# Kernel tuning notes

Hardware: AMD Instinct MI355X
Metric: run time of the kernel (lower is better)

Reference implementation:

```python
import jax, jax.numpy as jnp
import numpy as np

CHW = (1, 256, 256)
NPH, NPW = 16, 16
NB = 8          # n_blocks
D = 384         # hidden_d
H = 6           # n_heads
DH = D // H     # d_head = 64
OUT = 4
PH, PW = CHW[1] // NPH, CHW[2] // NPW
IN_D = CHW[0] * PH * PW        # 256
S = NPH * NPW + 1              # 257 tokens (CLS + patches)
EPS = 1e-5                     # torch LayerNorm default


def positional_embeddings(seq_len, d):
    # matches get_positional_embeddings: sin(i/10000^(j/d)) even j, cos(i/10000^((j-1)/d)) odd j
    i = jnp.arange(seq_len, dtype=jnp.float32)[:, None]
    j = jnp.arange(d, dtype=jnp.float32)[None, :]
    j_eff = jnp.where(j % 2 == 0, j, j - 1)
    ang = i / jnp.power(jnp.float32(10000.0), j_eff / d)
    return jnp.where(j % 2 == 0, jnp.sin(ang), jnp.cos(ang))


def patchify(images):
    # (n,c,h,w) -> (n, NPH*NPW, c*PH*PW), patch flattened channel-first like patch.flatten()
    n, c, h, w = images.shape
    x = images.reshape(n, c, NPH, PH, NPW, PW)
    x = x.transpose(0, 2, 4, 1, 3, 5)  # n, nph, npw, c, ph, pw
    return x.reshape(n, NPH * NPW, c * PH * PW)


def layernorm(x, g, b):
    mu = jnp.mean(x, axis=-1, keepdims=True)
    var = jnp.mean(jnp.square(x - mu), axis=-1, keepdims=True)
    return (x - mu) * jax.lax.rsqrt(var + EPS) * g + b


def mhsa(x, Wq, bq, Wk, bk, Wv, bv):
    # x: [B,S,D]; W*: [H,DH,DH] (torch Linear convention out=x@W.T+b), b*: [H,DH]
    B = x.shape[0]
    xh = x.reshape(B, S, H, DH)
    q = jnp.einsum('bshd,hed->bshe', xh, Wq) + bq
    k = jnp.einsum('bshd,hed->bshe', xh, Wk) + bk
    v = jnp.einsum('bshd,hed->bshe', xh, Wv) + bv
    scores = jnp.einsum('bqhe,bkhe->bhqk', q, k) / jnp.float32(DH) ** 0.5
    attn = jax.nn.softmax(scores, axis=-1)
    o = jnp.einsum('bhqk,bkhe->bqhe', attn, v)
    return o.reshape(B, S, D)


def setup_inputs() -> dict:
    key = jax.random.key(0)
    ks = jax.random.split(key, 24)
    s = 0.02
    B = 64
    inp = {
        'images': jax.random.normal(ks[0], (B, *CHW), jnp.float32),
        'Wmap': jax.random.normal(ks[1], (D, IN_D), jnp.float32) * s,
        'bmap': jax.random.normal(ks[2], (D,), jnp.float32) * s,
        'cls': jax.random.uniform(ks[3], (1, D), jnp.float32),
        'ln1_g': jnp.ones((NB, D), jnp.float32),
        'ln1_b': jnp.zeros((NB, D), jnp.float32),
        'Wq': jax.random.normal(ks[4], (NB, H, DH, DH), jnp.float32) * s,
        'bq': jax.random.normal(ks[5], (NB, H, DH), jnp.float32) * s,
        'Wk': jax.random.normal(ks[6], (NB, H, DH, DH), jnp.float32) * s,
        'bk': jax.random.normal(ks[7], (NB, H, DH), jnp.float32) * s,
        'Wv': jax.random.normal(ks[8], (NB, H, DH, DH), jnp.float32) * s,
        'bv': jax.random.normal(ks[9], (NB, H, DH), jnp.float32) * s,
        'ln2_g': jnp.ones((NB, D), jnp.float32),
        'ln2_b': jnp.zeros((NB, D), jnp.float32),
        'W1': jax.random.normal(ks[10], (NB, 4 * D, D), jnp.float32) * s,
        'b1': jax.random.normal(ks[11], (NB, 4 * D), jnp.float32) * s,
        'W2': jax.random.normal(ks[12], (NB, D, 4 * D), jnp.float32) * s,
        'b2': jax.random.normal(ks[13], (NB, D), jnp.float32) * s,
        'Wout': jax.random.normal(ks[14], (OUT, D), jnp.float32) * s,
        'bout': jax.random.normal(ks[15], (OUT,), jnp.float32) * s,
    }
    return inp


def reference(images, Wmap, bmap, cls, ln1_g, ln1_b, Wq, bq, Wk, bk, Wv, bv,
              ln2_g, ln2_b, W1, b1, W2, b2, Wout, bout):
    B = images.shape[0]
    patches = patchify(images)                        # [B, S-1, IN_D]
    tokens = patches @ Wmap.T + bmap                  # [B, S-1, D]
    tokens = jnp.concatenate([jnp.broadcast_to(cls[None], (B, 1, D)), tokens], axis=1)
    out = tokens + positional_embeddings(S, D)[None]  # [B, S, D]
    for blk in range(NB):
        out = out + mhsa(layernorm(out, ln1_g[blk], ln1_b[blk]),
                         Wq[blk], bq[blk], Wk[blk], bk[blk], Wv[blk], bv[blk])
        h = layernorm(out, ln2_g[blk], ln2_b[blk])
        h = jax.nn.gelu(h @ W1[blk].T + b1[blk], approximate=False)
        out = out + (h @ W2[blk].T + b2[blk])
    cls_out = out[:, 0]                               # [B, D]
    return jax.nn.softmax(cls_out @ Wout.T + bout, axis=-1)
```

## Files before the change

kernel.cpp:

```cpp
#include <hip/hip_runtime.h>

typedef __bf16 bf16x8 __attribute__((ext_vector_type(8)));
typedef float f32x4 __attribute__((ext_vector_type(4)));
typedef unsigned short u16;
typedef unsigned short u16x4 __attribute__((ext_vector_type(4)));

typedef __attribute__((address_space(3))) unsigned int as3_u32;
typedef __attribute__((address_space(1))) unsigned int as1_u32;

static __device__ __forceinline__ float b2f(u16 u) {
    union { unsigned int ui; float f; } v; v.ui = ((unsigned int)u) << 16; return v.f;
}
static __device__ __forceinline__ u16 f2b(float f) {
    union { float f; unsigned int u; } v; v.f = f;
    unsigned int r = v.u + 0x7FFFu + ((v.u >> 16) & 1u);
    return (u16)(r >> 16);
}
static __device__ __forceinline__ float h2f(u16 u) {
    union { u16 u; _Float16 h; } v; v.u = u; return (float)v.h;
}
static __device__ __forceinline__ u16 f2h(float f) {
    union { u16 u; _Float16 h; } v; v.h = (_Float16)f; return v.u;
}
static __device__ __forceinline__ float pos_emb(int s, int d) {
    int je = d & ~1;
    float ang = (float)s * powf(10000.0f, -(float)je / 384.0f);
    return (d & 1) ? cosf(ang) : sinf(ang);
}
static __device__ __forceinline__ float gelu_f(float x) {
    float xs = x * 0.70710678118654752f;
    float ax = fabsf(xs);
    float t = __builtin_amdgcn_rcpf(1.0f + 0.3275911f * ax);
    float poly = ((((1.061405429f * t - 1.453152027f) * t + 1.421413741f) * t
                   - 0.284496736f) * t + 0.254829592f) * t;
    float e = __expf(-ax * ax);
    float erfv = 1.0f - poly * e;
    erfv = (xs < 0.f) ? -erfv : erfv;
    return 0.5f * x * (1.0f + erfv);
}
static __device__ __forceinline__ void async16(const void* g, void* l) {
    __builtin_amdgcn_global_load_lds((const as1_u32*)g, (as3_u32*)l, 16, 0, 0);
}

#define MFMA16 __builtin_amdgcn_mfma_f32_16x16x32_bf16

static __device__ __forceinline__ bf16x8 ln8(const u16* __restrict__ p, float mu, float rs,
                                             f32x4 g0, f32x4 g1, f32x4 b0, f32x4 b1) {
    u16x4 xlo = *(const u16x4*)p;
    u16x4 xhi = *(const u16x4*)(p + 4);
    u16 o[8];
#pragma unroll
    for (int j = 0; j < 4; j++) o[j]     = f2b((h2f(xlo[j]) - mu) * rs * g0[j] + b0[j]);
#pragma unroll
    for (int j = 0; j < 4; j++) o[4 + j] = f2b((h2f(xhi[j]) - mu) * rs * g1[j] + b1[j]);
    return *(bf16x8*)o;
}

template<int K>
static __device__ __forceinline__ void stage_tile(const u16* __restrict__ gbase,
                                                  u16* lds, int kt, int t) {
#pragma unroll
    for (int j = 0; j < 4; j++) {
        int o = j * 4096 + t * 16;
        int row = o >> 7;
        int c = (o >> 4) & 7;
        int gc = c ^ (row & 7);
        const u16* src = gbase + (size_t)row * K + kt * 64 + gc * 8;
        async16(src, (char*)lds + o);
    }
}

template<int K, int EPI>
__global__ __launch_bounds__(256) void k_gemm128(const u16* __restrict__ A,
                                                 const u16* __restrict__ Bw,
                                                 const float* __restrict__ bias,
                                                 u16* __restrict__ out16,
                                                 u16* __restrict__ xres) {
    __shared__ u16 lds[2][128 * 64];
    const int t = threadIdx.x;
    const int NY = gridDim.y;
    int nwg = gridDim.x * NY;
    int flat = blockIdx.x + gridDim.x * blockIdx.y;
    int q8 = nwg >> 3, r8 = nwg & 7, xcd = flat & 7, idx = flat >> 3;
    int wg = (xcd < r8 ? xcd * (q8 + 1) : r8 * (q8 + 1) + (xcd - r8) * q8) + idx;
    const int mt = wg / NY, nt = wg - mt * NY;

    const u16* Ab = A + (size_t)mt * 128 * K;
    const u16* Bb = Bw + (size_t)nt * 128 * K;
    constexpr int NKT = K / 64;
    const int lane = t & 63, w = t >> 6;
    const int wm = (w >> 1) * 64, wn = (w & 1) * 64;
    const int r = lane & 15, g = lane >> 4;

    f32x4 acc[4][4] = {};
    for (int kt = 0; kt < NKT; kt++) {
        stage_tile<K>(Ab, lds[0], kt, t);
        stage_tile<K>(Bb, lds[1], kt, t);
        asm volatile("s_waitcnt vmcnt(0)" ::: "memory");
        __builtin_amdgcn_sched_barrier(0);
        __builtin_amdgcn_s_barrier();
        __builtin_amdgcn_sched_barrier(0);
#pragma unroll
        for (int ks = 0; ks < 2; ks++) {
            bf16x8 a[4], b[4];
#pragma unroll
            for (int i = 0; i < 4; i++) {
                int ra = wm + i * 16 + r;
                int ca = (ks * 4 + g) ^ (ra & 7);
                a[i] = *(const bf16x8*)((const char*)lds[0] + ra * 128 + ca * 16);
                int rb = wn + i * 16 + r;
                int cb = (ks * 4 + g) ^ (rb & 7);
                b[i] = *(const bf16x8*)((const char*)lds[1] + rb * 128 + cb * 16);
            }
            __builtin_amdgcn_s_setprio(1);
#pragma unroll
            for (int i = 0; i < 4; i++)
#pragma unroll
                for (int jj = 0; jj < 4; jj++)
                    acc[i][jj] = MFMA16(a[i], b[jj], acc[i][jj], 0, 0, 0);
            __builtin_amdgcn_s_setprio(0);
        }
        __builtin_amdgcn_s_barrier();
    }
#pragma unroll
    for (int i = 0; i < 4; i++) {
#pragma unroll
        for (int q = 0; q < 4; q++) {
            int ml = mt * 128 + wm + i * 16 + g * 4 + q;
#pragma unroll
            for (int jj = 0; jj < 4; jj++) {
                int n = nt * 128 + wn + jj * 16 + r;
                float v = acc[i][jj][q] + bias[n];
                if (EPI == 0) {
                    out16[(size_t)ml * 1536 + n] = f2b(gelu_f(v));
                } else {
                    if (ml < 16448) {
                        size_t o = (size_t)ml * 384 + n;
                        xres[o] = f2h(h2f(xres[o]) + v);
                    }
                }
            }
        }
    }
}

__global__ __launch_bounds__(64) void k_fattn(const u16* __restrict__ qb,
                                              const u16* __restrict__ kb,
                                              const u16* __restrict__ vT,
                                              u16* __restrict__ ao) {
    __shared__ u16 pl[32][40];
    const int lane = threadIdx.x;
    int flat = blockIdx.x;
    int xcd = flat & 7, idx = flat >> 3;
    int lbh = idx / 9;
    const int bh = xcd * 48 + lbh;
    const int q0 = (idx - lbh * 9) * 32;
    const int b = bh / 6, h = bh - b * 6;
    const int r = lane & 15, g = lane >> 4;

    const u16* qbase = qb + ((size_t)b * 257) * 384 + h * 64;
    const u16* kbase = kb + ((size_t)b * 257) * 384 + h * 64;
    const u16* vbase = vT + ((size_t)bh * 64) * 288;

    bf16x8 qf[2][2];
#pragma unroll
    for (int ti = 0; ti < 2; ti++)
#pragma unroll
        for (int kh = 0; kh < 2; kh++)
            qf[ti][kh] = *(const bf16x8*)(qbase + (size_t)(q0 + ti * 16 + r) * 384 + kh * 32 + g * 8);

    f32x4 accO[2][2][2] = {};
    f32x4 sum_[2] = {};

    for (int kv0 = 0; kv0 < 288; kv0 += 32) {
        bf16x8 kf[2][2];
#pragma unroll
        for (int tj = 0; tj < 2; tj++)
#pragma unroll
            for (int kh = 0; kh < 2; kh++)
                kf[tj][kh] = *(const bf16x8*)(kbase + (size_t)(kv0 + tj * 16 + r) * 384 + kh * 32 + g * 8);
        bf16x8 vf[2][2];
#pragma unroll
        for (int eT = 0; eT < 2; eT++)
#pragma unroll
            for (int tjE = 0; tjE < 2; tjE++)
                vf[eT][tjE] = *(const bf16x8*)(vbase + (size_t)(eT * 32 + tjE * 16 + r) * 288 + kv0 + g * 8);

        f32x4 s_[2][2] = {};
#pragma unroll
        for (int ti = 0; ti < 2; ti++)
#pragma unroll
            for (int tj = 0; tj < 2; tj++) {
                s_[ti][tj] = MFMA16(qf[ti][0], kf[tj][0], s_[ti][tj], 0, 0, 0);
                s_[ti][tj] = MFMA16(qf[ti][1], kf[tj][1], s_[ti][tj], 0, 0, 0);
            }
#pragma unroll
        for (int ti = 0; ti < 2; ti++) {
#pragma unroll
            for (int tj = 0; tj < 2; tj++) {
                bool bad = (kv0 + tj * 16 + r) >= 257;
#pragma unroll
                for (int q = 0; q < 4; q++) {
                    float p = bad ? 0.f : __expf(s_[ti][tj][q] * 0.125f);
                    s_[ti][tj][q] = p;
                }
                sum_[ti] += s_[ti][tj];
#pragma unroll
                for (int q = 0; q < 4; q++)
                    pl[ti * 16 + g * 4 + q][tj * 16 + r] = f2b(s_[ti][tj][q]);
            }
        }
        bf16x8 pa[2];
#pragma unroll
        for (int ti2 = 0; ti2 < 2; ti2++)
            pa[ti2] = *(const bf16x8*)&pl[ti2 * 16 + r][g * 8];
#pragma unroll
        for (int eT = 0; eT < 2; eT++)
#pragma unroll
            for (int ti2 = 0; ti2 < 2; ti2++)
#pragma unroll
                for (int tjE = 0; tjE < 2; tjE++)
                    accO[eT][ti2][tjE] = MFMA16(pa[ti2], vf[eT][tjE], accO[eT][ti2][tjE], 0, 0, 0);
    }
#pragma unroll
    for (int o = 1; o < 16; o <<= 1)
#pragma unroll
        for (int ti = 0; ti < 2; ti++)
#pragma unroll
            for (int q = 0; q < 4; q++)
                sum_[ti][q] += __shfl_xor(sum_[ti][q], o, 64);
#pragma unroll
    for (int ti = 0; ti < 2; ti++)
#pragma unroll
        for (int q = 0; q < 4; q++) {
            int qi = q0 + ti * 16 + g * 4 + q;
            if (qi < 257) {
                float inv = 1.0f / sum_[ti][q];
                u16* pao = ao + ((size_t)b * 257 + qi) * 384 + h * 64;
#pragma unroll
                for (int eT = 0; eT < 2; eT++)
#pragma unroll
                    for (int tjE = 0; tjE < 2; tjE++)
                        pao[eT * 32 + tjE * 16 + r] = f2b(accO[eT][ti][tjE][q] * inv);
            }
        }
}

__global__ __launch_bounds__(256) void k_cvt16(const void* __restrict__ src, u16* __restrict__ dst,
                                               int n, const unsigned* __restrict__ probe) {
    const bool isf32 = (*probe == 0x3F800000u);
    int i0 = (blockIdx.x * 256 + threadIdx.x) * 4;
    if (isf32) {
        const float* s = (const float*)src;
#pragma unroll
        for (int j = 0; j < 4; j++) { int i = i0 + j; if (i < n) dst[i] = f2b(s[i]); }
    } else {
        const u16* s = (const u16*)src;
#pragma unroll
        for (int j = 0; j < 4; j++) { int i = i0 + j; if (i < n) dst[i] = s[i]; }
    }
}
__global__ __launch_bounds__(256) void k_cvt32(const void* __restrict__ src, float* __restrict__ dst,
                                               int n, const unsigned* __restrict__ probe) {
    const bool isf32 = (*probe == 0x3F800000u);
    int i0 = (blockIdx.x * 256 + threadIdx.x) * 4;
    if (isf32) {
        const float* s = (const float*)src;
#pragma unroll
        for (int j = 0; j < 4; j++) { int i = i0 + j; if (i < n) dst[i] = s[i]; }
    } else {
        const u16* s = (const u16*)src;
#pragma unroll
        for (int j = 0; j < 4; j++) { int i = i0 + j; if (i < n) dst[i] = b2f(s[i]); }
    }
}

__global__ __launch_bounds__(256) void k_vtpad(u16* __restrict__ vT) {
    int idx = blockIdx.x * 256 + threadIdx.x;
    const int total = 384 * 64 * 31;
    if (idx < total) {
        int be = idx / 31; int s = 257 + (idx - be * 31);
        vT[(size_t)be * 288 + s] = 0;
    }
}

__global__ __launch_bounds__(256) void k_patch(const u16* __restrict__ img,
                                               const u16* __restrict__ Wmap,
                                               const float* __restrict__ bmap,
                                               u16* __restrict__ x) {
    const int lane = threadIdx.x & 63;
    const int wv = threadIdx.x >> 6;
    const int mt = blockIdx.x * 4 + wv;
    const int nt = blockIdx.y;
    const int m0 = mt * 32, n0 = nt * 32;
    const int r = lane & 15, kr = (lane >> 4) << 3;
    f32x4 acc[2][2] = {};
    int ma = m0 + r;
    size_t base0 = (size_t)(ma >> 8) * 65536 + (size_t)((ma >> 4) & 15) * 4096 + (size_t)(ma & 15) * 16;
    ma += 16;
    size_t base1 = (size_t)(ma >> 8) * 65536 + (size_t)((ma >> 4) & 15) * 4096 + (size_t)(ma & 15) * 16;
    const u16* pb0 = Wmap + (size_t)(n0 + r) * 256 + kr;
    const u16* pb1 = pb0 + 16 * 256;
    for (int k0 = 0; k0 < 256; k0 += 32) {
        int k = k0 + kr;
        size_t off = (size_t)(k >> 4) * 256 + (k & 15);
        bf16x8 a0 = *(const bf16x8*)(img + base0 + off);
        bf16x8 a1 = *(const bf16x8*)(img + base1 + off);
        bf16x8 b0 = *(const bf16x8*)(pb0 + k0);
        bf16x8 b1 = *(const bf16x8*)(pb1 + k0);
        acc[0][0] = MFMA16(a0, b0, acc[0][0], 0, 0, 0);
        acc[0][1] = MFMA16(a0, b1, acc[0][1], 0, 0, 0);
        acc[1][0] = MFMA16(a1, b0, acc[1][0], 0, 0, 0);
        acc[1][1] = MFMA16(a1, b1, acc[1][1], 0, 0, 0);
    }
#pragma unroll
    for (int ti = 0; ti < 2; ti++)
#pragma unroll
        for (int i = 0; i < 4; i++) {
            int m = m0 + ti * 16 + ((lane >> 4) << 2) + i;
            int b = m >> 8, p = m & 255, s = p + 1;
            u16* px = x + ((size_t)b * 257 + s) * 384;
#pragma unroll
            for (int tj = 0; tj < 2; tj++) {
                int n = n0 + tj * 16 + (lane & 15);
                px[n] = f2h(acc[ti][tj][i] + bmap[n] + pos_emb(s, n));
            }
        }
}

__global__ __launch_bounds__(384) void k_cls(const float* __restrict__ cls, u16* __restrict__ x) {
    int b = blockIdx.x, d = threadIdx.x;
    x[(size_t)b * 257 * 384 + d] = f2h(cls[d] + pos_emb(0, d));
}

__global__ __launch_bounds__(256) void k_stats(const u16* __restrict__ x,
                                               float* __restrict__ st) {
    const int lane = threadIdx.x & 63, wv = threadIdx.x >> 6;
    const int row = blockIdx.x * 16 + wv * 4 + (lane >> 4);
    const int r = lane & 15;
    const u16* px = x + (size_t)row * 384;
    f32x4 v[6]; float s = 0.f;
#pragma unroll
    for (int i = 0; i < 6; i++) {
        u16x4 x4 = *(const u16x4*)(px + i * 64 + r * 4);
#pragma unroll
        for (int j = 0; j < 4; j++) v[i][j] = h2f(x4[j]);
        s += v[i][0] + v[i][1] + v[i][2] + v[i][3];
    }
#pragma unroll
    for (int o = 1; o < 16; o <<= 1) s += __shfl_xor(s, o, 64);
    float mu = s * (1.0f / 384.0f);
    float q = 0.f;
#pragma unroll
    for (int i = 0; i < 6; i++)
#pragma unroll
        for (int j = 0; j < 4; j++) { float d = v[i][j] - mu; q += d * d; }
#pragma unroll
    for (int o = 1; o < 16; o <<= 1) q += __shfl_xor(q, o, 64);
    float rstd = rsqrtf(q * (1.0f / 384.0f) + 1e-5f);
    if (r == 0) { st[row * 2] = mu; st[row * 2 + 1] = rstd; }
}

__global__ __launch_bounds__(256) void k_ln2r(u16* __restrict__ x,
                                              const u16* __restrict__ ao,
                                              const float* __restrict__ g,
                                              const float* __restrict__ bb,
                                              u16* __restrict__ xn) {
    const int lane = threadIdx.x & 63, wv = threadIdx.x >> 6;
    const int row = blockIdx.x * 16 + wv * 4 + (lane >> 4);
    const int r = lane & 15;
    u16* px = x + (size_t)row * 384;
    const u16* pa = ao + (size_t)row * 384;
    f32x4 v[6]; float s = 0.f;
#pragma unroll
    for (int i = 0; i < 6; i++) {
        u16x4 x4 = *(const u16x4*)(px + i * 64 + r * 4);
        u16x4 a4 = *(const u16x4*)(pa + i * 64 + r * 4);
#pragma unroll
        for (int j = 0; j < 4; j++) v[i][j] = h2f(x4[j]) + b2f(a4[j]);
        s += v[i][0] + v[i][1] + v[i][2] + v[i][3];
    }
#pragma unroll
    for (int o = 1; o < 16; o <<= 1) s += __shfl_xor(s, o, 64);
    float mu = s * (1.0f / 384.0f);
    float q = 0.f;
#pragma unroll
    for (int i = 0; i < 6; i++)
#pragma unroll
        for (int j = 0; j < 4; j++) { float d = v[i][j] - mu; q += d * d; }
#pragma unroll
    for (int o = 1; o < 16; o <<= 1) q += __shfl_xor(q, o, 64);
    float rstd = rsqrtf(q * (1.0f / 384.0f) + 1e-5f);
    u16* po = xn + (size_t)row * 384;
#pragma unroll
    for (int i = 0; i < 6; i++) {
        int d0 = i * 64 + r * 4;
        u16x4 h4;
#pragma unroll
        for (int j = 0; j < 4; j++) h4[j] = f2h(v[i][j]);
        *(u16x4*)(px + d0) = h4;
        f32x4 gg = *(const f32x4*)(g + d0);
        f32x4 bv = *(const f32x4*)(bb + d0);
        u16x4 o4;
#pragma unroll
        for (int j = 0; j < 4; j++) o4[j] = f2b((v[i][j] - mu) * rstd * gg[j] + bv[j]);
        *(u16x4*)(po + d0) = o4;
    }
}

__global__ __launch_bounds__(256) void k_qkv3(const u16* __restrict__ x,
                                              const float* __restrict__ st,
                                              const float* __restrict__ lg,
                                              const float* __restrict__ lb,
                                              const u16* __restrict__ Wq,
                                              const u16* __restrict__ Wk,
                                              const u16* __restrict__ Wv,
                                              const float* __restrict__ bq,
                                              const float* __restrict__ bk,
                                              const float* __restrict__ bv,
                                              u16* __restrict__ qo,
                                              u16* __restrict__ ko,
                                              u16* __restrict__ vT) {
    const int lane = threadIdx.x & 63, wv = threadIdx.x >> 6;
    int nwg = 129 * 12;
    int flat = blockIdx.x + 129 * blockIdx.y;
    int q8 = nwg >> 3, r8 = nwg & 7, xcd = flat & 7, idx = flat >> 3;
    int wg = (xcd < r8 ? xcd * (q8 + 1) : r8 * (q8 + 1) + (xcd - r8) * q8) + idx;
    int bxx = wg / 12, rest = wg - bxx * 12;

    const int mt = bxx * 4 + wv; if (mt >= 514) return;
    const int nt = rest & 1, h = rest >> 1;
    const int r = lane & 15, kr = (lane >> 4) << 3;

    const int row0 = mt * 32 + r, row1 = row0 + 16;
    const u16* xr0 = x + (size_t)row0 * 384 + h * 64;
    const u16* xr1 = x + (size_t)row1 * 384 + h * 64;
    const float mu0 = st[row0 * 2], rs0 = st[row0 * 2 + 1];
    const float mu1 = st[row1 * 2], rs1 = st[row1 * 2 + 1];
    f32x4 gA = *(const f32x4*)(lg + h * 64 + kr);
    f32x4 gB = *(const f32x4*)(lg + h * 64 + kr + 4);
    f32x4 gC = *(const f32x4*)(lg + h * 64 + 32 + kr);
    f32x4 gD = *(const f32x4*)(lg + h * 64 + 32 + kr + 4);
    f32x4 bA = *(const f32x4*)(lb + h * 64 + kr);
    f32x4 bB = *(const f32x4*)(lb + h * 64 + kr + 4);
    f32x4 bC = *(const f32x4*)(lb + h * 64 + 32 + kr);
    f32x4 bD = *(const f32x4*)(lb + h * 64 + 32 + kr + 4);

    bf16x8 a00 = ln8(xr0 + kr, mu0, rs0, gA, gB, bA, bB);
    bf16x8 a10 = ln8(xr1 + kr, mu1, rs1, gA, gB, bA, bB);
    bf16x8 a01 = ln8(xr0 + 32 + kr, mu0, rs0, gC, gD, bC, bD);
    bf16x8 a11 = ln8(xr1 + 32 + kr, mu1, rs1, gC, gD, bC, bD);

    const u16* Ws[3] = { Wq, Wk, Wv };
    const float* bs[3] = { bq, bk, bv };
#pragma unroll
    for (int ty = 0; ty < 3; ty++) {
        const u16* Bb = Ws[ty] + ((size_t)h * 64 + nt * 32) * 64;
        bf16x8 b00 = *(const bf16x8*)(Bb + (size_t)r * 64 + kr);
        bf16x8 b10 = *(const bf16x8*)(Bb + (size_t)(16 + r) * 64 + kr);
        bf16x8 b01 = *(const bf16x8*)(Bb + (size_t)r * 64 + 32 + kr);
        bf16x8 b11 = *(const bf16x8*)(Bb + (size_t)(16 + r) * 64 + 32 + kr);
        f32x4 acc[2][2] = {};
        acc[0][0] = MFMA16(a00, b00, acc[0][0], 0, 0, 0);
        acc[0][1] = MFMA16(a00, b10, acc[0][1], 0, 0, 0);
        acc[1][0] = MFMA16(a10, b00, acc[1][0], 0, 0, 0);
        acc[1][1] = MFMA16(a10, b10, acc[1][1], 0, 0, 0);
        acc[0][0] = MFMA16(a01, b01, acc[0][0], 0, 0, 0);
        acc[0][1] = MFMA16(a01, b11, acc[0][1], 0, 0, 0);
        acc[1][0] = MFMA16(a11, b01, acc[1][0], 0, 0, 0);
        acc[1][1] = MFMA16(a11, b11, acc[1][1], 0, 0, 0);
        const float* bias = bs[ty];
#pragma unroll
        for (int ti = 0; ti < 2; ti++)
#pragma unroll
            for (int i = 0; i < 4; i++) {
                int m = mt * 32 + ti * 16 + ((lane >> 4) << 2) + i;
#pragma unroll
                for (int tj = 0; tj < 2; tj++) {
                    int nl = nt * 32 + tj * 16 + (lane & 15);
                    float v = acc[ti][tj][i] + bias[h * 64 + nl];
                    if (ty == 0) {
                        qo[(size_t)m * 384 + h * 64 + nl] = f2b(v);
                    } else if (ty == 1) {
                        ko[(size_t)m * 384 + h * 64 + nl] = f2b(v);
                    } else {
                        int b = m / 257, s = m - b * 257;
                        vT[(((size_t)b * 6 + h) * 64 + nl) * 288 + s] = f2b(v);
                    }
                }
            }
    }
}

__global__ __launch_bounds__(256) void k_head(const u16* __restrict__ x,
                                              const float* __restrict__ Wout,
                                              const float* __restrict__ bout,
                                              float* __restrict__ out) {
    int t = threadIdx.x; int b = t >> 2, o = t & 3;
    const u16* px = x + (size_t)b * 257 * 384;
    const float* pw = Wout + o * 384;
    float s = 0.f;
    for (int d = 0; d < 384; d++) s += h2f(px[d]) * pw[d];
    s += bout[o];
    float mx = fmaxf(s, __shfl_xor(s, 1, 4));
    mx = fmaxf(mx, __shfl_xor(mx, 2, 4));
    float e = expf(s - mx);
    float sm = e + __shfl_xor(e, 1, 4);
    sm += __shfl_xor(sm, 2, 4);
    out[t] = e / sm;
}

extern "C" void kernel_launch(void* const* d_in, const int* in_sizes, int n_in,
                              void* d_out, int out_size, void* d_ws, size_t ws_size,
                              hipStream_t stream) {
    const unsigned* probe = (const unsigned*)d_in[4];

    char* w = (char*)d_ws;
    size_t used = 0;
    auto alloc = [&](size_t bytes) -> char* {
        char* p = w + used; used += (bytes + 255) & ~(size_t)255; return p;
    };
    u16*   x   = (u16*)  alloc(16448ull * 384 * 2);
    u16*   xn  = (u16*)  alloc(16512ull * 384 * 2);
    u16*   qb  = (u16*)  alloc(16448ull * 384 * 2);
    u16*   kb  = (u16*)  alloc(16448ull * 384 * 2);
    u16*   vT  = (u16*)  alloc(384ull * 64 * 288 * 2);
    u16*   ao  = (u16*)  alloc(16448ull * 384 * 2);
    float* stx = (float*)alloc(16448ull * 2 * 4);
    u16*   imB = (u16*)  alloc(4194304ull * 2);
    u16*   WmB = (u16*)  alloc(98304ull * 2);
    u16*   WqB = (u16*)  alloc(196608ull * 2);
    u16*   WkB = (u16*)  alloc(196608ull * 2);
    u16*   WvB = (u16*)  alloc(196608ull * 2);
    u16*   W1B = (u16*)  alloc(4718592ull * 2);
    u16*   W2B = (u16*)  alloc(4718592ull * 2);
    float* prm = (float*)alloc(39172ull * 4);
    u16*   hb  = (u16*)  alloc(16512ull * 1536 * 2);
    (void)ws_size;

    float* bmapF = prm + 0;
    float* clsF  = prm + 384;
    float* ln1gF = prm + 768;
    float* ln1bF = prm + 3840;
    float* bqF   = prm + 6912;
    float* bkF   = prm + 9984;
    float* bvF   = prm + 13056;
    float* ln2gF = prm + 16128;
    float* ln2bF = prm + 19200;
    float* b1F   = prm + 22272;
    float* b2F   = prm + 34560;
    float* WoutF = prm + 37632;
    float* boutF = prm + 39168;

    dim3 B256(256);
    auto cvt16 = [&](const void* src, u16* dst, int n) {
        hipLaunchKernelGGL(k_cvt16, dim3((n + 1023) / 1024), B256, 0, stream, src, dst, n, probe);
    };
    auto cvt32 = [&](const void* src, float* dst, int n) {
        hipLaunchKernelGGL(k_cvt32, dim3((n + 1023) / 1024), B256, 0, stream, src, dst, n, probe);
    };
    cvt16(d_in[0],  imB, 4194304);
    cvt16(d_in[1],  WmB, 98304);
    cvt16(d_in[6],  WqB, 196608);
    cvt16(d_in[8],  WkB, 196608);
    cvt16(d_in[10], WvB, 196608);
    cvt16(d_in[14], W1B, 4718592);
    cvt16(d_in[16], W2B, 4718592);
    cvt32(d_in[2],  bmapF, 384);
    cvt32(d_in[3],  clsF,  384);
    cvt32(d_in[4],  ln1gF, 3072);
    cvt32(d_in[5],  ln1bF, 3072);
    cvt32(d_in[7],  bqF,   3072);
    cvt32(d_in[9],  bkF,   3072);
    cvt32(d_in[11], bvF,   3072);
    cvt32(d_in[12], ln2gF, 3072);
    cvt32(d_in[13], ln2bF, 3072);
    cvt32(d_in[15], b1F,   12288);
    cvt32(d_in[17], b2F,   3072);
    cvt32(d_in[18], WoutF, 1536);
    cvt32(d_in[19], boutF, 4);
    (void)in_sizes; (void)n_in; (void)out_size;

    hipMemsetAsync(xn + 16448ull * 384, 0, 64ull * 384 * 2, stream);

    hipLaunchKernelGGL(k_vtpad, dim3((384 * 64 * 31 + 255) / 256), B256, 0, stream, vT);
    hipLaunchKernelGGL(k_patch, dim3(128, 12), B256, 0, stream, imB, WmB, bmapF, x);
    hipLaunchKernelGGL(k_cls, dim3(64), dim3(384), 0, stream, clsF, x);
    for (int blk = 0; blk < 8; blk++) {
        hipLaunchKernelGGL(k_stats, dim3(1028), B256, 0, stream, x, stx);
        hipLaunchKernelGGL(k_qkv3, dim3(129, 12), B256, 0, stream, x, stx,
                           ln1gF + blk * 384, ln1bF + blk * 384,
                           WqB + (size_t)blk * 24576, WkB + (size_t)blk * 24576, WvB + (size_t)blk * 24576,
                           bqF + blk * 384, bkF + blk * 384, bvF + blk * 384,
                           qb, kb, vT);
        hipLaunchKernelGGL(k_fattn, dim3(3456), dim3(64), 0, stream, qb, kb, vT, ao);
        hipLaunchKernelGGL(k_ln2r, dim3(1028), B256, 0, stream, x, ao,
                           ln2gF + blk * 384, ln2bF + blk * 384, xn);
        k_gemm128<384, 0><<<dim3(129, 12), B256, 0, stream>>>(
            xn, W1B + (size_t)blk * 1536 * 384, b1F + blk * 1536, hb, nullptr);
        k_gemm128<1536, 1><<<dim3(129, 3), B256, 0, stream>>>(
            hb, W2B + (size_t)blk * 384 * 1536, b2F + blk * 384, nullptr, x);
    }
    hipLaunchKernelGGL(k_head, dim3(1), B256, 0, stream, x, WoutF, boutF, (float*)d_out);
}
```

Measured before the change: 1.341 ms.

## Compute only CLS token rows in the final transformer block

In the last block only the CLS token's output feeds the classification head. The attention query side, LN2+residual, and the MLP are therefore restricted to the 64 CLS rows through a CLS-mode attention launch, a small ln2 kernel writing a compact buffer, and a new GEMM epilogue that scatters back to the CLS rows. K/V for all tokens are still computed, so attention remains exact. This cuts roughly seven-eighths of the last block's attention-output and MLP work but adds code paths and a padded compact buffer.

```diff
diff --git a/kernel.cpp b/kernel.cpp
--- a/kernel.cpp
+++ b/kernel.cpp
@@ -133,9 +133,14 @@
                 float v = acc[i][jj][q] + bias[n];
                 if (EPI == 0) {
                     out16[(size_t)ml * 1536 + n] = f2b(gelu_f(v));
-                } else {
+                } else if (EPI == 1) {
                     if (ml < 16448) {
                         size_t o = (size_t)ml * 384 + n;
+                        xres[o] = f2h(h2f(xres[o]) + v);
+                    }
+                } else {
+                    if (ml < 64) {
+                        size_t o = ((size_t)ml * 257) * 384 + n;
                         xres[o] = f2h(h2f(xres[o]) + v);
                     }
                 }
@@ -147,14 +152,19 @@
 __global__ __launch_bounds__(64) void k_fattn(const u16* __restrict__ qb,
                                               const u16* __restrict__ kb,
                                               const u16* __restrict__ vT,
-                                              u16* __restrict__ ao) {
+                                              u16* __restrict__ ao, int clsmode) {
     __shared__ u16 pl[32][40];
     const int lane = threadIdx.x;
     int flat = blockIdx.x;
-    int xcd = flat & 7, idx = flat >> 3;
-    int lbh = idx / 9;
-    const int bh = xcd * 48 + lbh;
-    const int q0 = (idx - lbh * 9) * 32;
+    int bh, q0;
+    if (clsmode) {
+        bh = flat; q0 = 0;
+    } else {
+        int xcd = flat & 7, idx = flat >> 3;
+        int lbh = idx / 9;
+        bh = xcd * 48 + lbh;
+        q0 = (idx - lbh * 9) * 32;
+    }
     const int b = bh / 6, h = bh - b * 6;
     const int r = lane & 15, g = lane >> 4;
 
@@ -408,6 +418,54 @@
     }
 }
 
+__global__ __launch_bounds__(256) void k_ln2r_cls(u16* __restrict__ x,
+                                                  const u16* __restrict__ ao,
+                                                  const float* __restrict__ g,
+                                                  const float* __restrict__ bb,
+                                                  u16* __restrict__ xnc) {
+    const int lane = threadIdx.x & 63, wv = threadIdx.x >> 6;
+    const int bi = blockIdx.x * 16 + wv * 4 + (lane >> 4);
+    const int r = lane & 15;
+    const size_t row = (size_t)bi * 257;
+    u16* px = x + row * 384;
+    const u16* pa = ao + row * 384;
+    f32x4 v[6]; float s = 0.f;
+#pragma unroll
+    for (int i = 0; i < 6; i++) {
+        u16x4 x4 = *(const u16x4*)(px + i * 64 + r * 4);
+        u16x4 a4 = *(const u16x4*)(pa + i * 64 + r * 4);
+#pragma unroll
+        for (int j = 0; j < 4; j++) v[i][j] = h2f(x4[j]) + b2f(a4[j]);
+        s += v[i][0] + v[i][1] + v[i][2] + v[i][3];
+    }
+#pragma unroll
+    for (int o = 1; o < 16; o <<= 1) s += __shfl_xor(s, o, 64);
+    float mu = s * (1.0f / 384.0f);
+    float q = 0.f;
+#pragma unroll
+    for (int i = 0; i < 6; i++)
+#pragma unroll
+        for (int j = 0; j < 4; j++) { float d = v[i][j] - mu; q += d * d; }
+#pragma unroll
+    for (int o = 1; o < 16; o <<= 1) q += __shfl_xor(q, o, 64);
+    float rstd = rsqrtf(q * (1.0f / 384.0f) + 1e-5f);
+    u16* po = xnc + (size_t)bi * 384;
+#pragma unroll
+    for (int i = 0; i < 6; i++) {
+        int d0 = i * 64 + r * 4;
+        u16x4 h4;
+#pragma unroll
+        for (int j = 0; j < 4; j++) h4[j] = f2h(v[i][j]);
+        *(u16x4*)(px + d0) = h4;
+        f32x4 gg = *(const f32x4*)(g + d0);
+        f32x4 bv = *(const f32x4*)(bb + d0);
+        u16x4 o4;
+#pragma unroll
+        for (int j = 0; j < 4; j++) o4[j] = f2b((v[i][j] - mu) * rstd * gg[j] + bv[j]);
+        *(u16x4*)(po + d0) = o4;
+    }
+}
+
 __global__ __launch_bounds__(256) void k_qkv3(const u16* __restrict__ x,
                                               const float* __restrict__ st,
                                               const float* __restrict__ lg,
@@ -522,6 +580,7 @@
     };
     u16*   x   = (u16*)  alloc(16448ull * 384 * 2);
     u16*   xn  = (u16*)  alloc(16512ull * 384 * 2);
+    u16*   xnc = (u16*)  alloc(128ull * 384 * 2);
     u16*   qb  = (u16*)  alloc(16448ull * 384 * 2);
     u16*   kb  = (u16*)  alloc(16448ull * 384 * 2);
     u16*   vT  = (u16*)  alloc(384ull * 64 * 288 * 2);
@@ -582,6 +641,7 @@
     (void)in_sizes; (void)n_in; (void)out_size;
 
     hipMemsetAsync(xn + 16448ull * 384, 0, 64ull * 384 * 2, stream);
+    hipMemsetAsync(xnc + 64ull * 384, 0, 64ull * 384 * 2, stream);
 
     hipLaunchKernelGGL(k_vtpad, dim3((384 * 64 * 31 + 255) / 256), B256, 0, stream, vT);
     hipLaunchKernelGGL(k_patch, dim3(128, 12), B256, 0, stream, imB, WmB, bmapF, x);
@@ -593,13 +653,23 @@
                            WqB + (size_t)blk * 24576, WkB + (size_t)blk * 24576, WvB + (size_t)blk * 24576,
                            bqF + blk * 384, bkF + blk * 384, bvF + blk * 384,
                            qb, kb, vT);
-        hipLaunchKernelGGL(k_fattn, dim3(3456), dim3(64), 0, stream, qb, kb, vT, ao);
-        hipLaunchKernelGGL(k_ln2r, dim3(1028), B256, 0, stream, x, ao,
-                           ln2gF + blk * 384, ln2bF + blk * 384, xn);
-        k_gemm128<384, 0><<<dim3(129, 12), B256, 0, stream>>>(
-            xn, W1B + (size_t)blk * 1536 * 384, b1F + blk * 1536, hb, nullptr);
-        k_gemm128<1536, 1><<<dim3(129, 3), B256, 0, stream>>>(
-            hb, W2B + (size_t)blk * 384 * 1536, b2F + blk * 384, nullptr, x);
+        if (blk < 7) {
+            hipLaunchKernelGGL(k_fattn, dim3(3456), dim3(64), 0, stream, qb, kb, vT, ao, 0);
+            hipLaunchKernelGGL(k_ln2r, dim3(1028), B256, 0, stream, x, ao,
+                               ln2gF + blk * 384, ln2bF + blk * 384, xn);
+            k_gemm128<384, 0><<<dim3(129, 12), B256, 0, stream>>>(
+                xn, W1B + (size_t)blk * 1536 * 384, b1F + blk * 1536, hb, nullptr);
+            k_gemm128<1536, 1><<<dim3(129, 3), B256, 0, stream>>>(
+                hb, W2B + (size_t)blk * 384 * 1536, b2F + blk * 384, nullptr, x);
+        } else {
+            hipLaunchKernelGGL(k_fattn, dim3(384), dim3(64), 0, stream, qb, kb, vT, ao, 1);
+            hipLaunchKernelGGL(k_ln2r_cls, dim3(4), B256, 0, stream, x, ao,
+                               ln2gF + blk * 384, ln2bF + blk * 384, xnc);
+            k_gemm128<384, 0><<<dim3(1, 12), B256, 0, stream>>>(
+                xnc, W1B + (size_t)blk * 1536 * 384, b1F + blk * 1536, hb, nullptr);
+            k_gemm128<1536, 2><<<dim3(1, 3), B256, 0, stream>>>(
+                hb, W2B + (size_t)blk * 384 * 1536, b2F + blk * 384, nullptr, x);
+        }
     }
     hipLaunchKernelGGL(k_head, dim3(1), B256, 0, stream, x, WoutF, boutF, (float*)d_out);
 }
```

Result: faster. 1.282 ms (-4.4%).
